# Kernel optimization log

Hardware: AMD Instinct MI355X
Metric: run time of the kernel (lower is better)

The kernel has to match this reference:

```python
import jax, jax.numpy as jnp
import numpy as np

B, P, K, H, W = 32, 8, 17, 192, 192
ALPHA = 0.5
TEMP = 2.0
SIGMA = 3.0


def _bce_with_logits_mean(x, t):
    # numerically stable BCEWithLogitsLoss, reduction='mean'
    return jnp.mean(jnp.maximum(x, 0.0) - x * t + jnp.log1p(jnp.exp(-jnp.abs(x))))


def _kl_batchmean(s_logprob, t_prob):
    # torch KLDivLoss(reduction='batchmean'): sum(t * (log t - log s)) / batch
    return jnp.sum(t_prob * (jnp.log(t_prob) - s_logprob)) / s_logprob.shape[0]


def _keypoints_loss(pred, kps, vis):
    # pred: [B,K,H,W]; kps: [B,P,K,2] normalized; vis: [B,P,K] int
    b, k, h, w = pred.shape
    x = jnp.floor(kps[..., 0] * (w - 1))  # [B,P,K]; coords>=0 so floor == int()
    y = jnp.floor(kps[..., 1] * (h - 1))
    valid = ((vis > 0) & (x >= 0) & (x < w) & (y >= 0) & (y < h)).astype(pred.dtype)
    inv2s2 = 1.0 / (2.0 * SIGMA * SIGMA)
    ax = jnp.arange(w, dtype=pred.dtype)
    ay = jnp.arange(h, dtype=pred.dtype)
    # separable Gaussian: exp(-((a-x)^2+(b-y)^2)/2s^2) = gx(a)*gy(b)
    gx = jnp.exp(-(ax - x[..., None]) ** 2 * inv2s2) * valid[..., None]  # [B,P,K,W]
    gy = jnp.exp(-(ay - y[..., None]) ** 2 * inv2s2)                     # [B,P,K,H]
    # original indexes target[k][a,b] with a over grid_x (W axis); H==W required
    target = jnp.einsum('bpkw,bpkh->bkwh', gx, gy)  # [B,K,W,H] == [B,K,H,W]
    per = jnp.sum((pred - target) ** 2, axis=(1, 2, 3))          # F.mse_loss sum
    denom = jnp.sum(vis, axis=(1, 2)).astype(pred.dtype) + 1e-6
    return jnp.mean(per / denom)


def setup_inputs() -> dict:
    key = jax.random.key(0)
    k1, k2, k3, k4, k5, k6, k7 = jax.random.split(key, 7)
    return {
        's_seg_logits': jax.random.normal(k1, (B, 1, H, W), dtype=jnp.float32),
        's_pose_logits': jax.random.normal(k2, (B, K, H, W), dtype=jnp.float32),
        't_seg_logits': jax.random.normal(k3, (B, 1, H, W), dtype=jnp.float32),
        't_pose_logits': jax.random.normal(k4, (B, K, H, W), dtype=jnp.float32),
        'mask': jax.random.uniform(k5, (B, H, W), dtype=jnp.float32),
        'keypoints': jax.random.uniform(k6, (B, P, K, 2), dtype=jnp.float32),
        'visibilities': jax.random.randint(k7, (B, P, K), 0, 2, dtype=jnp.int32),
    }


def reference(s_seg_logits, s_pose_logits, t_seg_logits, t_pose_logits, mask, keypoints, visibilities):
    # task losses
    task_seg = _bce_with_logits_mean(s_seg_logits, mask[:, None])  # unsqueeze(1)
    task_pose = _keypoints_loss(s_pose_logits, keypoints, visibilities)
    task_loss = task_seg + task_pose
    # segmentation distillation (softmax over channel dim)
    s_seg_lp = jax.nn.log_softmax(s_seg_logits / TEMP, axis=1)
    t_seg_p = jax.nn.softmax(t_seg_logits / TEMP, axis=1)
    seg_distill = _kl_batchmean(s_seg_lp, t_seg_p) * TEMP ** 2
    # pose distillation (softmax over flattened K*H*W)
    s_pose_lp = jax.nn.log_softmax(s_pose_logits.reshape(s_pose_logits.shape[0], -1) / TEMP, axis=1)
    t_pose_p = jax.nn.softmax(t_pose_logits.reshape(t_pose_logits.shape[0], -1) / TEMP, axis=1)
    pose_distill = _kl_batchmean(s_pose_lp, t_pose_p) * TEMP ** 2
    distill_loss = seg_distill + pose_distill
    total = ALPHA * distill_loss + (1.0 - ALPHA) * task_loss
    return total
```

## Files before the change

kernel.cpp:

```cpp
#include <hip/hip_runtime.h>
#include <math.h>

#define B_   32
#define P_   8
#define K_   17
#define H_   192
#define W_   192
#define HW_  (H_*W_)
#define PB4   156672
#define NBLKS 2048
#define PER_B_BLKS 64
#define CHUNK 16384
#define FULL_IT 9
#define REM4  9216
#define BCE4  294912

#define KPU  (K_*P_)
#define TSQ_UNITS   (B_*K_)
#define RADIUS 18

#define WS_BLK   0
#define WS_STAMP 16384
#define WS_TSQ   20736

typedef __attribute__((ext_vector_type(4))) float f4v;

__device__ inline f4v ntload4(const float* p) {
    return __builtin_nontemporal_load((const f4v*)p);
}

__device__ inline float wave_red_sum(float v) {
    for (int o = 32; o; o >>= 1) v += __shfl_xor(v, o, 64);
    return v;
}

__device__ inline void kl_elem(float sv, float tv,
        float& S2, float& Zu, float& Zv, float& A) {
    S2 += sv*sv;
    float u = tv*0.5f, v = sv*0.5f;
    float eu = __expf(u);
    Zu += eu;
    A  += eu*(u - v);
    Zv += __expf(v);
}

__global__ void __launch_bounds__(256) main_kernel(
        const float* __restrict__ s_pose, const float* __restrict__ t_pose,
        const float* __restrict__ kps,    const int* __restrict__ vis,
        const float* __restrict__ s_seg,  const float* __restrict__ mask,
        float* __restrict__ ws) {
    __shared__ float sred[4][5];
    __shared__ float gx_s[40], gy_s[40];

    const int blk = blockIdx.x;
    const int tid = threadIdx.x;
    const float inv18 = 1.0f / 18.0f;

    const int b  = blk >> 6;
    const int lg = ((blk & 63) << 8) | tid;
    const float* s4 = s_pose + ((size_t)b*PB4 + lg)*4;
    const float* t4 = t_pose + ((size_t)b*PB4 + lg)*4;

    float S2 = 0.f, Zu = 0.f, Zv = 0.f, A = 0.f;
#pragma unroll 3
    for (int j = 0; j < FULL_IT; j++) {
        f4v sv = ntload4(s4 + (size_t)j*CHUNK*4);
        f4v tv = ntload4(t4 + (size_t)j*CHUNK*4);
        kl_elem(sv.x, tv.x, S2, Zu, Zv, A);
        kl_elem(sv.y, tv.y, S2, Zu, Zv, A);
        kl_elem(sv.z, tv.z, S2, Zu, Zv, A);
        kl_elem(sv.w, tv.w, S2, Zu, Zv, A);
    }
    if (lg < REM4) {
        f4v sv = ntload4(s4 + (size_t)FULL_IT*CHUNK*4);
        f4v tv = ntload4(t4 + (size_t)FULL_IT*CHUNK*4);
        kl_elem(sv.x, tv.x, S2, Zu, Zv, A);
        kl_elem(sv.y, tv.y, S2, Zu, Zv, A);
        kl_elem(sv.z, tv.z, S2, Zu, Zv, A);
        kl_elem(sv.w, tv.w, S2, Zu, Zv, A);
    }

    float bce = 0.f;
    {
        int gid = (blk << 8) | tid;
        if (gid < BCE4) {
            f4v xv = ntload4(s_seg + (size_t)gid*4);
            f4v mv = ntload4(mask  + (size_t)gid*4);
            bce += fmaxf(xv.x, 0.f) - xv.x*mv.x + log1pf(__expf(-fabsf(xv.x)));
            bce += fmaxf(xv.y, 0.f) - xv.y*mv.y + log1pf(__expf(-fabsf(xv.y)));
            bce += fmaxf(xv.z, 0.f) - xv.z*mv.z + log1pf(__expf(-fabsf(xv.z)));
            bce += fmaxf(xv.w, 0.f) - xv.w*mv.w + log1pf(__expf(-fabsf(xv.w)));
        }
    }

    S2  = wave_red_sum(S2);
    Zu  = wave_red_sum(Zu);
    Zv  = wave_red_sum(Zv);
    A   = wave_red_sum(A);
    bce = wave_red_sum(bce);
    {
        int w = tid >> 6;
        if ((tid & 63) == 0) {
            sred[w][0] = S2; sred[w][1] = Zu; sred[w][2] = Zv;
            sred[w][3] = A;  sred[w][4] = bce;
        }
    }
    __syncthreads();
    if (tid == 0) {
        float* o = ws + WS_BLK + (size_t)blk * 8;
#pragma unroll
        for (int c = 0; c < 5; c++)
            o[c] = sred[0][c] + sred[1][c] + sred[2][c] + sred[3][c];
    }

    for (int j = blk & 63; j < KPU; j += 64) {
        __syncthreads();
        int u   = b*KPU + j;
        int kk  = j / P_;
        int pp  = j - kk*P_;
        float kx = kps[((b*P_ + pp)*K_ + kk)*2 + 0];
        float ky = kps[((b*P_ + pp)*K_ + kk)*2 + 1];
        int   vv = vis[(b*P_ + pp)*K_ + kk];
        float fx = floorf(kx * 191.f);
        float fy = floorf(ky * 191.f);
        bool ok = (vv > 0) && fx >= 0.f && fx < 192.f && fy >= 0.f && fy < 192.f;
        float acc = 0.f;
        if (ok) {
            int X0 = max(0, (int)fx - RADIUS), X1 = min(H_-1, (int)fx + RADIUS);
            int Y0 = max(0, (int)fy - RADIUS), Y1 = min(W_-1, (int)fy + RADIUS);
            int nr = X1 - X0 + 1, nc = Y1 - Y0 + 1;
            if (tid < nr) {
                float d = (float)(X0 + tid) - fx;
                gx_s[tid] = __expf(-d*d*inv18);
            } else if (tid >= 64 && tid - 64 < nc) {
                float d = (float)(Y0 + tid - 64) - fy;
                gy_s[tid - 64] = __expf(-d*d*inv18);
            }
            __syncthreads();
            const float* pb = s_pose + (size_t)(b*K_ + kk) * HW_;
            int lim = nr << 6;
            for (int e = tid; e < lim; e += 256) {
                int row = e >> 6, col = e & 63;
                if (col < nc)
                    acc += pb[(X0 + row)*W_ + (Y0 + col)] * gx_s[row] * gy_s[col];
            }
        }
        acc = wave_red_sum(acc);
        if ((tid & 63) == 0) sred[tid >> 6][0] = acc;
        __syncthreads();
        if (tid == 0)
            ws[WS_STAMP + u] = sred[0][0] + sred[1][0] + sred[2][0] + sred[3][0];
    }

    if (blk < TSQ_UNITS) {
        __syncthreads();
        int bb = blk / K_, kk = blk - bb*K_;
        int pq = tid >> 2, p = pq >> 3, q = pq & 7, ln = tid & 3;
        float kxp = kps[((bb*P_ + p)*K_ + kk)*2 + 0];
        float kyp = kps[((bb*P_ + p)*K_ + kk)*2 + 1];
        float kxq = kps[((bb*P_ + q)*K_ + kk)*2 + 0];
        float kyq = kps[((bb*P_ + q)*K_ + kk)*2 + 1];
        int vp = vis[(bb*P_ + p)*K_ + kk];
        int vq = vis[(bb*P_ + q)*K_ + kk];
        float axp = floorf(kxp * 191.f), ayp = floorf(kyp * 191.f);
        float axq = floorf(kxq * 191.f), ayq = floorf(kyq * 191.f);
        bool okp = (vp > 0) && axp >= 0.f && axp < 192.f && ayp >= 0.f && ayp < 192.f;
        bool okq = (vq > 0) && axq >= 0.f && axq < 192.f && ayq >= 0.f && ayq < 192.f;
        float sx = 0.f, sy = 0.f;
        int i0 = ln * 48;
        for (int i = i0; i < i0 + 48; i++) {
            float da = (float)i - axp, db = (float)i - axq;
            sx += __expf(-(da*da + db*db)*inv18);
            float ea = (float)i - ayp, eb = (float)i - ayq;
            sy += __expf(-(ea*ea + eb*eb)*inv18);
        }
        sx += __shfl_xor(sx, 1, 64); sy += __shfl_xor(sy, 1, 64);
        sx += __shfl_xor(sx, 2, 64); sy += __shfl_xor(sy, 2, 64);
        float val = (ln == 0 && okp && okq) ? sx * sy : 0.f;
        val = wave_red_sum(val);
        if ((tid & 63) == 0) sred[tid >> 6][0] = val;
        __syncthreads();
        if (tid == 0)
            ws[WS_TSQ + blk] = sred[0][0] + sred[1][0] + sred[2][0] + sred[3][0];
    }
}

__global__ void __launch_bounds__(256) finalize_kernel(
        const float* __restrict__ ws, const int* __restrict__ vis,
        float* __restrict__ out) {
    __shared__ float rS2[B_][8], rZu[B_][8], rZv[B_][8], rA[B_][8];
    __shared__ float rCr[B_][8], rTq[B_][8];
    __shared__ int   rVs[B_][8];
    __shared__ float skl[B_], skp[B_];
    __shared__ float bw[4];
    int tid = threadIdx.x;
    int b = tid >> 3, s = tid & 7;

    float S2 = 0.f, Zu = 0.f, Zv = 0.f, A = 0.f, cr = 0.f, tq = 0.f;
    for (int j = s; j < PER_B_BLKS; j += 8) {
        const float* p = ws + WS_BLK + (size_t)(b*PER_B_BLKS + j) * 8;
        S2 += p[0]; Zu += p[1]; Zv += p[2]; A += p[3];
    }
    for (int j = s; j < KPU; j += 8) cr += ws[WS_STAMP + b*KPU + j];
    for (int j = s; j < K_;  j += 8) tq += ws[WS_TSQ + b*K_ + j];
    int vs = 0;
    for (int m = s; m < P_*K_; m += 8) vs += vis[b*(P_*K_) + m];
    rS2[b][s] = S2; rZu[b][s] = Zu; rZv[b][s] = Zv; rA[b][s] = A;
    rCr[b][s] = cr; rTq[b][s] = tq; rVs[b][s] = vs;

    float bce = 0.f;
    for (int i = tid; i < NBLKS; i += 256)
        bce += ws[WS_BLK + (size_t)i * 8 + 4];
    bce = wave_red_sum(bce);
    if ((tid & 63) == 0) bw[tid >> 6] = bce;
    __syncthreads();

    if (tid < B_) {
        float tS2=0.f, tZu=0.f, tZv=0.f, tA=0.f, tCr=0.f, tTq=0.f; int tVs=0;
#pragma unroll
        for (int q2 = 0; q2 < 8; q2++) {
            tS2 += rS2[tid][q2]; tZu += rZu[tid][q2]; tZv += rZv[tid][q2];
            tA  += rA[tid][q2];  tCr += rCr[tid][q2]; tTq += rTq[tid][q2];
            tVs += rVs[tid][q2];
        }
        float mse = tS2 - 2.f*tCr + tTq;
        skl[tid] = tA/tZu + (logf(tZv) - logf(tZu));
        skp[tid] = mse / ((float)tVs + 1e-6f);
    }
    __syncthreads();

    if (tid == 0) {
        float kl = 0.f, kpv = 0.f;
        for (int i = 0; i < B_; i++) { kl += skl[i]; kpv += skp[i]; }
        float bsum = bw[0] + bw[1] + bw[2] + bw[3];
        float pose_distill = 4.0f * kl / (float)B_;
        float task_seg  = bsum / (float)(B_ * HW_);
        float task_pose = kpv / (float)B_;
        out[0] = 0.5f * pose_distill + 0.5f * (task_seg + task_pose);
    }
}

extern "C" void kernel_launch(void* const* d_in, const int* in_sizes, int n_in,
                              void* d_out, int out_size, void* d_ws, size_t ws_size,
                              hipStream_t stream) {
    const float* s_seg  = (const float*)d_in[0];
    const float* s_pose = (const float*)d_in[1];
    const float* t_pose = (const float*)d_in[3];
    const float* mask   = (const float*)d_in[4];
    const float* kps    = (const float*)d_in[5];
    const int*   vis    = (const int*)d_in[6];
    float* out = (float*)d_out;
    float* ws  = (float*)d_ws;

    main_kernel<<<NBLKS, 256, 0, stream>>>(s_pose, t_pose, kps, vis,
                                           s_seg, mask, ws);
    finalize_kernel<<<1, 256, 0, stream>>>(ws, vis, out);
}
```

Measured before the change: 206.2 us.

## Fuse finalize into main kernel via last-block counter and wave-per-stamp

Merges the finalize kernel into the main kernel using an atomic arrival counter so the last block performs the final reduction. The keypoint stamp correlation now uses one wave per (k,p) unit with per-lane column Gaussians and batched row loads, instead of looping whole blocks. The tsq work is spread across blocks, nontemporal loads become ordinary loads, and an occupancy hint is added. A memset is added to reset the counter, and correctness now depends on the fence/atomic ordering.

```diff
diff --git a/kernel.cpp b/kernel.cpp
--- a/kernel.cpp
+++ b/kernel.cpp
@@ -16,18 +16,14 @@
 #define BCE4  294912
 
 #define KPU  (K_*P_)
-#define TSQ_UNITS   (B_*K_)
 #define RADIUS 18
 
 #define WS_BLK   0
 #define WS_STAMP 16384
 #define WS_TSQ   20736
+#define WS_CNT   7
 
 typedef __attribute__((ext_vector_type(4))) float f4v;
-
-__device__ inline f4v ntload4(const float* p) {
-    return __builtin_nontemporal_load((const f4v*)p);
-}
 
 __device__ inline float wave_red_sum(float v) {
     for (int o = 32; o; o >>= 1) v += __shfl_xor(v, o, 64);
@@ -44,13 +40,18 @@
     Zv += __expf(v);
 }
 
-__global__ void __launch_bounds__(256) main_kernel(
+__global__ void __launch_bounds__(256, 8) main_kernel(
         const float* __restrict__ s_pose, const float* __restrict__ t_pose,
         const float* __restrict__ kps,    const int* __restrict__ vis,
         const float* __restrict__ s_seg,  const float* __restrict__ mask,
-        float* __restrict__ ws) {
+        float* __restrict__ ws, float* __restrict__ out) {
     __shared__ float sred[4][5];
-    __shared__ float gx_s[40], gy_s[40];
+    __shared__ float rS2[B_][8], rZu[B_][8], rZv[B_][8], rA[B_][8];
+    __shared__ float rCr[B_][8], rTq[B_][8];
+    __shared__ int   rVs[B_][8];
+    __shared__ float skl[B_], skp[B_];
+    __shared__ float bw4[4];
+    __shared__ int   is_last;
 
     const int blk = blockIdx.x;
     const int tid = threadIdx.x;
@@ -58,22 +59,22 @@
 
     const int b  = blk >> 6;
     const int lg = ((blk & 63) << 8) | tid;
-    const float* s4 = s_pose + ((size_t)b*PB4 + lg)*4;
-    const float* t4 = t_pose + ((size_t)b*PB4 + lg)*4;
+    const f4v* s4 = (const f4v*)s_pose + (size_t)b*PB4 + lg;
+    const f4v* t4 = (const f4v*)t_pose + (size_t)b*PB4 + lg;
 
     float S2 = 0.f, Zu = 0.f, Zv = 0.f, A = 0.f;
 #pragma unroll 3
     for (int j = 0; j < FULL_IT; j++) {
-        f4v sv = ntload4(s4 + (size_t)j*CHUNK*4);
-        f4v tv = ntload4(t4 + (size_t)j*CHUNK*4);
+        f4v sv = s4[(size_t)j*CHUNK];
+        f4v tv = t4[(size_t)j*CHUNK];
         kl_elem(sv.x, tv.x, S2, Zu, Zv, A);
         kl_elem(sv.y, tv.y, S2, Zu, Zv, A);
         kl_elem(sv.z, tv.z, S2, Zu, Zv, A);
         kl_elem(sv.w, tv.w, S2, Zu, Zv, A);
     }
     if (lg < REM4) {
-        f4v sv = ntload4(s4 + (size_t)FULL_IT*CHUNK*4);
-        f4v tv = ntload4(t4 + (size_t)FULL_IT*CHUNK*4);
+        f4v sv = s4[(size_t)FULL_IT*CHUNK];
+        f4v tv = t4[(size_t)FULL_IT*CHUNK];
         kl_elem(sv.x, tv.x, S2, Zu, Zv, A);
         kl_elem(sv.y, tv.y, S2, Zu, Zv, A);
         kl_elem(sv.z, tv.z, S2, Zu, Zv, A);
@@ -84,8 +85,8 @@
     {
         int gid = (blk << 8) | tid;
         if (gid < BCE4) {
-            f4v xv = ntload4(s_seg + (size_t)gid*4);
-            f4v mv = ntload4(mask  + (size_t)gid*4);
+            f4v xv = ((const f4v*)s_seg)[gid];
+            f4v mv = ((const f4v*)mask)[gid];
             bce += fmaxf(xv.x, 0.f) - xv.x*mv.x + log1pf(__expf(-fabsf(xv.x)));
             bce += fmaxf(xv.y, 0.f) - xv.y*mv.y + log1pf(__expf(-fabsf(xv.y)));
             bce += fmaxf(xv.z, 0.f) - xv.z*mv.z + log1pf(__expf(-fabsf(xv.z)));
@@ -113,130 +114,138 @@
             o[c] = sred[0][c] + sred[1][c] + sred[2][c] + sred[3][c];
     }
 
-    for (int j = blk & 63; j < KPU; j += 64) {
+    {
+        const int wv = tid >> 6, lane = tid & 63;
+        const int lw = ((blk & 63) << 2) | wv;
+        if (lw < KPU) {
+            int kk = lw >> 3, pp = lw & 7;
+            int ki = (b*P_ + pp)*K_ + kk;
+            float kx = kps[ki*2 + 0];
+            float ky = kps[ki*2 + 1];
+            int   vv = vis[ki];
+            float fx = floorf(kx * 191.f);
+            float fy = floorf(ky * 191.f);
+            bool ok = (vv > 0) && fx >= 0.f && fx < 192.f && fy >= 0.f && fy < 192.f;
+            float acc = 0.f;
+            if (ok) {
+                int X0 = max(0, (int)fx - RADIUS), X1 = min(H_-1, (int)fx + RADIUS);
+                int Y0 = max(0, (int)fy - RADIUS), Y1 = min(W_-1, (int)fy + RADIUS);
+                int nr = X1 - X0 + 1, nc = Y1 - Y0 + 1;
+                float gy_l = 0.f;
+                if (lane < nc) {
+                    float d = (float)(Y0 + lane) - fy;
+                    gy_l = __expf(-d*d*inv18);
+                }
+                const float* pb = s_pose + (size_t)(b*K_ + kk)*HW_ + Y0 + lane;
+                float racc = 0.f;
+                for (int r0 = 0; r0 < nr; r0 += 8) {
+                    float vbuf[8];
+#pragma unroll
+                    for (int u = 0; u < 8; u++) {
+                        int r = r0 + u;
+                        vbuf[u] = (r < nr && lane < nc) ? pb[(size_t)(X0 + r)*W_] : 0.f;
+                    }
+#pragma unroll
+                    for (int u = 0; u < 8; u++) {
+                        float d = (float)(X0 + r0 + u) - fx;
+                        racc += vbuf[u] * __expf(-d*d*inv18);
+                    }
+                }
+                acc = racc * gy_l;
+            }
+            acc = wave_red_sum(acc);
+            if (lane == 0) ws[WS_STAMP + b*KPU + lw] = acc;
+        }
+    }
+
+    {
+        int kk4 = blk & 63;
+        if (kk4 < K_) {
+            __syncthreads();
+            int pq = tid >> 2, p = pq >> 3, q = pq & 7, ln = tid & 3;
+            float kxp = kps[((b*P_ + p)*K_ + kk4)*2 + 0];
+            float kyp = kps[((b*P_ + p)*K_ + kk4)*2 + 1];
+            float kxq = kps[((b*P_ + q)*K_ + kk4)*2 + 0];
+            float kyq = kps[((b*P_ + q)*K_ + kk4)*2 + 1];
+            int vp = vis[(b*P_ + p)*K_ + kk4];
+            int vq = vis[(b*P_ + q)*K_ + kk4];
+            float axp = floorf(kxp * 191.f), ayp = floorf(kyp * 191.f);
+            float axq = floorf(kxq * 191.f), ayq = floorf(kyq * 191.f);
+            bool okp = (vp > 0) && axp >= 0.f && axp < 192.f && ayp >= 0.f && ayp < 192.f;
+            bool okq = (vq > 0) && axq >= 0.f && axq < 192.f && ayq >= 0.f && ayq < 192.f;
+            float sx = 0.f, sy = 0.f;
+            int i0 = ln * 48;
+            for (int i = i0; i < i0 + 48; i++) {
+                float da = (float)i - axp, db = (float)i - axq;
+                sx += __expf(-(da*da + db*db)*inv18);
+                float ea = (float)i - ayp, eb = (float)i - ayq;
+                sy += __expf(-(ea*ea + eb*eb)*inv18);
+            }
+            sx += __shfl_xor(sx, 1, 64); sy += __shfl_xor(sy, 1, 64);
+            sx += __shfl_xor(sx, 2, 64); sy += __shfl_xor(sy, 2, 64);
+            float val = (ln == 0 && okp && okq) ? sx * sy : 0.f;
+            val = wave_red_sum(val);
+            if ((tid & 63) == 0) sred[tid >> 6][0] = val;
+            __syncthreads();
+            if (tid == 0)
+                ws[WS_TSQ + b*K_ + kk4] = sred[0][0] + sred[1][0] + sred[2][0] + sred[3][0];
+        }
+    }
+
+    __syncthreads();
+    if (tid == 0) {
+        __threadfence();
+        unsigned prev = __hip_atomic_fetch_add((unsigned*)(ws + WS_CNT), 1u,
+                            __ATOMIC_ACQ_REL, __HIP_MEMORY_SCOPE_AGENT);
+        is_last = (prev == NBLKS - 1);
+    }
+    __syncthreads();
+    if (!is_last) return;
+
+    {
+        int b2 = tid >> 3, s = tid & 7;
+        float fS2 = 0.f, fZu = 0.f, fZv = 0.f, fA = 0.f, cr = 0.f, tq = 0.f;
+        for (int j = s; j < PER_B_BLKS; j += 8) {
+            const float* p = ws + WS_BLK + (size_t)(b2*PER_B_BLKS + j) * 8;
+            fS2 += p[0]; fZu += p[1]; fZv += p[2]; fA += p[3];
+        }
+        for (int j = s; j < KPU; j += 8) cr += ws[WS_STAMP + b2*KPU + j];
+        for (int j = s; j < K_;  j += 8) tq += ws[WS_TSQ + b2*K_ + j];
+        int vsum = 0;
+        for (int m = s; m < P_*K_; m += 8) vsum += vis[b2*(P_*K_) + m];
+        rS2[b2][s] = fS2; rZu[b2][s] = fZu; rZv[b2][s] = fZv; rA[b2][s] = fA;
+        rCr[b2][s] = cr;  rTq[b2][s] = tq;  rVs[b2][s] = vsum;
+
+        float bce2 = 0.f;
+        for (int i = tid; i < NBLKS; i += 256)
+            bce2 += ws[WS_BLK + (size_t)i * 8 + 4];
+        bce2 = wave_red_sum(bce2);
+        if ((tid & 63) == 0) bw4[tid >> 6] = bce2;
         __syncthreads();
-        int u   = b*KPU + j;
-        int kk  = j / P_;
-        int pp  = j - kk*P_;
-        float kx = kps[((b*P_ + pp)*K_ + kk)*2 + 0];
-        float ky = kps[((b*P_ + pp)*K_ + kk)*2 + 1];
-        int   vv = vis[(b*P_ + pp)*K_ + kk];
-        float fx = floorf(kx * 191.f);
-        float fy = floorf(ky * 191.f);
-        bool ok = (vv > 0) && fx >= 0.f && fx < 192.f && fy >= 0.f && fy < 192.f;
-        float acc = 0.f;
-        if (ok) {
-            int X0 = max(0, (int)fx - RADIUS), X1 = min(H_-1, (int)fx + RADIUS);
-            int Y0 = max(0, (int)fy - RADIUS), Y1 = min(W_-1, (int)fy + RADIUS);
-            int nr = X1 - X0 + 1, nc = Y1 - Y0 + 1;
-            if (tid < nr) {
-                float d = (float)(X0 + tid) - fx;
-                gx_s[tid] = __expf(-d*d*inv18);
-            } else if (tid >= 64 && tid - 64 < nc) {
-                float d = (float)(Y0 + tid - 64) - fy;
-                gy_s[tid - 64] = __expf(-d*d*inv18);
+
+        if (tid < B_) {
+            float tS2=0.f, tZu=0.f, tZv=0.f, tA=0.f, tCr=0.f, tTq=0.f; int tVs=0;
+#pragma unroll
+            for (int q2 = 0; q2 < 8; q2++) {
+                tS2 += rS2[tid][q2]; tZu += rZu[tid][q2]; tZv += rZv[tid][q2];
+                tA  += rA[tid][q2];  tCr += rCr[tid][q2]; tTq += rTq[tid][q2];
+                tVs += rVs[tid][q2];
             }
-            __syncthreads();
-            const float* pb = s_pose + (size_t)(b*K_ + kk) * HW_;
-            int lim = nr << 6;
-            for (int e = tid; e < lim; e += 256) {
-                int row = e >> 6, col = e & 63;
-                if (col < nc)
-                    acc += pb[(X0 + row)*W_ + (Y0 + col)] * gx_s[row] * gy_s[col];
-            }
-        }
-        acc = wave_red_sum(acc);
-        if ((tid & 63) == 0) sred[tid >> 6][0] = acc;
+            float mse = tS2 - 2.f*tCr + tTq;
+            skl[tid] = tA/tZu + (logf(tZv) - logf(tZu));
+            skp[tid] = mse / ((float)tVs + 1e-6f);
+        }
         __syncthreads();
-        if (tid == 0)
-            ws[WS_STAMP + u] = sred[0][0] + sred[1][0] + sred[2][0] + sred[3][0];
-    }
-
-    if (blk < TSQ_UNITS) {
-        __syncthreads();
-        int bb = blk / K_, kk = blk - bb*K_;
-        int pq = tid >> 2, p = pq >> 3, q = pq & 7, ln = tid & 3;
-        float kxp = kps[((bb*P_ + p)*K_ + kk)*2 + 0];
-        float kyp = kps[((bb*P_ + p)*K_ + kk)*2 + 1];
-        float kxq = kps[((bb*P_ + q)*K_ + kk)*2 + 0];
-        float kyq = kps[((bb*P_ + q)*K_ + kk)*2 + 1];
-        int vp = vis[(bb*P_ + p)*K_ + kk];
-        int vq = vis[(bb*P_ + q)*K_ + kk];
-        float axp = floorf(kxp * 191.f), ayp = floorf(kyp * 191.f);
-        float axq = floorf(kxq * 191.f), ayq = floorf(kyq * 191.f);
-        bool okp = (vp > 0) && axp >= 0.f && axp < 192.f && ayp >= 0.f && ayp < 192.f;
-        bool okq = (vq > 0) && axq >= 0.f && axq < 192.f && ayq >= 0.f && ayq < 192.f;
-        float sx = 0.f, sy = 0.f;
-        int i0 = ln * 48;
-        for (int i = i0; i < i0 + 48; i++) {
-            float da = (float)i - axp, db = (float)i - axq;
-            sx += __expf(-(da*da + db*db)*inv18);
-            float ea = (float)i - ayp, eb = (float)i - ayq;
-            sy += __expf(-(ea*ea + eb*eb)*inv18);
-        }
-        sx += __shfl_xor(sx, 1, 64); sy += __shfl_xor(sy, 1, 64);
-        sx += __shfl_xor(sx, 2, 64); sy += __shfl_xor(sy, 2, 64);
-        float val = (ln == 0 && okp && okq) ? sx * sy : 0.f;
-        val = wave_red_sum(val);
-        if ((tid & 63) == 0) sred[tid >> 6][0] = val;
-        __syncthreads();
-        if (tid == 0)
-            ws[WS_TSQ + blk] = sred[0][0] + sred[1][0] + sred[2][0] + sred[3][0];
-    }
-}
-
-__global__ void __launch_bounds__(256) finalize_kernel(
-        const float* __restrict__ ws, const int* __restrict__ vis,
-        float* __restrict__ out) {
-    __shared__ float rS2[B_][8], rZu[B_][8], rZv[B_][8], rA[B_][8];
-    __shared__ float rCr[B_][8], rTq[B_][8];
-    __shared__ int   rVs[B_][8];
-    __shared__ float skl[B_], skp[B_];
-    __shared__ float bw[4];
-    int tid = threadIdx.x;
-    int b = tid >> 3, s = tid & 7;
-
-    float S2 = 0.f, Zu = 0.f, Zv = 0.f, A = 0.f, cr = 0.f, tq = 0.f;
-    for (int j = s; j < PER_B_BLKS; j += 8) {
-        const float* p = ws + WS_BLK + (size_t)(b*PER_B_BLKS + j) * 8;
-        S2 += p[0]; Zu += p[1]; Zv += p[2]; A += p[3];
-    }
-    for (int j = s; j < KPU; j += 8) cr += ws[WS_STAMP + b*KPU + j];
-    for (int j = s; j < K_;  j += 8) tq += ws[WS_TSQ + b*K_ + j];
-    int vs = 0;
-    for (int m = s; m < P_*K_; m += 8) vs += vis[b*(P_*K_) + m];
-    rS2[b][s] = S2; rZu[b][s] = Zu; rZv[b][s] = Zv; rA[b][s] = A;
-    rCr[b][s] = cr; rTq[b][s] = tq; rVs[b][s] = vs;
-
-    float bce = 0.f;
-    for (int i = tid; i < NBLKS; i += 256)
-        bce += ws[WS_BLK + (size_t)i * 8 + 4];
-    bce = wave_red_sum(bce);
-    if ((tid & 63) == 0) bw[tid >> 6] = bce;
-    __syncthreads();
-
-    if (tid < B_) {
-        float tS2=0.f, tZu=0.f, tZv=0.f, tA=0.f, tCr=0.f, tTq=0.f; int tVs=0;
-#pragma unroll
-        for (int q2 = 0; q2 < 8; q2++) {
-            tS2 += rS2[tid][q2]; tZu += rZu[tid][q2]; tZv += rZv[tid][q2];
-            tA  += rA[tid][q2];  tCr += rCr[tid][q2]; tTq += rTq[tid][q2];
-            tVs += rVs[tid][q2];
-        }
-        float mse = tS2 - 2.f*tCr + tTq;
-        skl[tid] = tA/tZu + (logf(tZv) - logf(tZu));
-        skp[tid] = mse / ((float)tVs + 1e-6f);
-    }
-    __syncthreads();
-
-    if (tid == 0) {
-        float kl = 0.f, kpv = 0.f;
-        for (int i = 0; i < B_; i++) { kl += skl[i]; kpv += skp[i]; }
-        float bsum = bw[0] + bw[1] + bw[2] + bw[3];
-        float pose_distill = 4.0f * kl / (float)B_;
-        float task_seg  = bsum / (float)(B_ * HW_);
-        float task_pose = kpv / (float)B_;
-        out[0] = 0.5f * pose_distill + 0.5f * (task_seg + task_pose);
+
+        if (tid == 0) {
+            float kl = 0.f, kpv = 0.f;
+            for (int i = 0; i < B_; i++) { kl += skl[i]; kpv += skp[i]; }
+            float bsum = bw4[0] + bw4[1] + bw4[2] + bw4[3];
+            float pose_distill = 4.0f * kl / (float)B_;
+            float task_seg  = bsum / (float)(B_ * HW_);
+            float task_pose = kpv / (float)B_;
+            out[0] = 0.5f * pose_distill + 0.5f * (task_seg + task_pose);
+        }
     }
 }
 
@@ -252,7 +261,7 @@
     float* out = (float*)d_out;
     float* ws  = (float*)d_ws;
 
+    hipMemsetAsync((char*)d_ws + WS_CNT*sizeof(float), 0, sizeof(unsigned), stream);
     main_kernel<<<NBLKS, 256, 0, stream>>>(s_pose, t_pose, kps, vis,
-                                           s_seg, mask, ws);
-    finalize_kernel<<<1, 256, 0, stream>>>(ws, vis, out);
-}
+                                           s_seg, mask, ws, out);
+}
```

Result: slower. 358.9 us (+74.0%).
